# Kernel tuning notes

Measured on AMD Instinct MI355X. Metric: run time of the kernel, lower is better.

The kernel has to match this reference:

```python
import jax, jax.numpy as jnp
import numpy as np

B, C, H, W = 16, 256, 64, 64
DIM = 8
HEADS = C // DIM          # 32
TD = HEADS * DIM          # 256 (total_dim)
EPS = 1e-15
BN_EPS = 1e-5


def setup_inputs() -> dict:
    key = jax.random.key(0)
    ks = jax.random.split(key, 7)
    s = 0.05
    return {
        "x": jax.random.normal(ks[0], (B, C, H, W), jnp.float32),
        "w_qkv": jax.random.normal(ks[1], (3 * TD, C), jnp.float32) * s,
        "w_dw": jax.random.normal(ks[2], (3 * TD, 1, 5, 5), jnp.float32) * s,
        "w_pw": jax.random.normal(ks[3], (3 * TD, DIM), jnp.float32) * s,
        "w_proj": jax.random.normal(ks[4], (C, 2 * TD), jnp.float32) * s,
        "bn_gamma": jnp.ones((C,), jnp.float32),
        "bn_beta": jnp.zeros((C,), jnp.float32),
        "bn_mean": jax.random.normal(ks[5], (C,), jnp.float32) * 0.1,
        "bn_var": jax.random.uniform(ks[6], (C,), jnp.float32, 0.5, 1.5),
    }


def reference(x, w_qkv, w_dw, w_pw, w_proj, bn_gamma, bn_beta, bn_mean, bn_var):
    # qkv: 1x1 conv, no bias -> (B, 3*TD, H, W)
    qkv = jnp.einsum('bchw,oc->bohw', x, w_qkv)

    # multi-scale aggregation: 5x5 depthwise conv then grouped 1x1 conv (groups = 3*HEADS)
    dw = jax.lax.conv_general_dilated(
        qkv, w_dw, window_strides=(1, 1), padding=[(2, 2), (2, 2)],
        dimension_numbers=('NCHW', 'OIHW', 'NCHW'), feature_group_count=3 * TD)
    G = 3 * HEADS                                   # groups; DIM channels per group
    dwg = dw.reshape(B, G, DIM, H, W)
    wg = w_pw.reshape(G, DIM, DIM)                  # (group, out_per_group, in_per_group)
    agg = jnp.einsum('bgihw,goi->bgohw', dwg, wg).reshape(B, 3 * TD, H, W)

    qkv_ms = jnp.concatenate([qkv, agg], axis=1)    # (B, 6*TD, H, W)

    # ReLU linear attention (H*W > dim branch)
    h2 = qkv_ms.shape[1] // (3 * DIM)               # 2*HEADS effective heads
    t = qkv_ms.reshape(B, h2, 3 * DIM, H * W)
    q = jax.nn.relu(t[:, :, :DIM])                  # (B,h2,DIM,N)
    k = jax.nn.relu(t[:, :, DIM:2 * DIM])           # (B,h2,DIM,N)
    v = t[:, :, 2 * DIM:]                           # (B,h2,DIM,N)
    v = jnp.concatenate([v, jnp.ones_like(v[:, :, :1])], axis=2)  # pad ones row -> (B,h2,DIM+1,N)

    vk = jnp.einsum('bhen,bhdn->bhed', v, k)        # (B,h2,DIM+1,DIM)
    out = jnp.einsum('bhed,bhdn->bhen', vk, q)      # (B,h2,DIM+1,N)
    out = out[:, :, :-1] / (out[:, :, -1:] + EPS)   # normalize by padded-ones channel
    out = out.reshape(B, h2 * DIM, H, W)            # (B, 2*TD, H, W)

    # proj: 1x1 conv + BatchNorm (inference stats)
    y = jnp.einsum('bchw,oc->bohw', out, w_proj)
    scale = (bn_gamma / jnp.sqrt(bn_var + BN_EPS))[None, :, None, None]
    y = (y - bn_mean[None, :, None, None]) * scale + bn_beta[None, :, None, None]

    return x + y
```

## Files before the change

### kernel.cpp

```cpp
#include <hip/hip_runtime.h>

#define BB 16
#define CC 256
#define HW 4096
#define TD3 768
#define TD2 512
#define WQ_N (TD3 * CC)
#define WP_N (CC * TD2)

typedef __bf16 bf16x8 __attribute__((ext_vector_type(8)));
typedef float f32x4 __attribute__((ext_vector_type(4)));
typedef const __attribute__((address_space(1))) unsigned int glb_u32;
typedef __attribute__((address_space(3))) unsigned int lds_u32;

__device__ inline ushort f2bf(float f) {
    union { float f; uint u; } v; v.f = f;
    uint u = v.u;
    return (ushort)((u + 0x7FFFu + ((u >> 16) & 1u)) >> 16);
}
__device__ inline float bf2f(ushort h) {
    union { uint u; float f; } v; v.u = ((uint)h) << 16;
    return v.f;
}
__device__ inline uint pack2(float a, float b) {
    return (uint)f2bf(a) | ((uint)f2bf(b) << 16);
}

__launch_bounds__(256)
__global__ void k_prep(const float* __restrict__ w_qkv, const float* __restrict__ w_proj,
                       ushort* __restrict__ wq_hi, ushort* __restrict__ wq_lo,
                       ushort* __restrict__ wp_hi, ushort* __restrict__ wp_lo) {
    int i = blockIdx.x * 256 + threadIdx.x;
    if (i < WQ_N) {
        float f = w_qkv[i];
        ushort h = f2bf(f);
        wq_hi[i] = h;
        wq_lo[i] = f2bf(f - bf2f(h));
    }
    if (i < WP_N) {
        float f = w_proj[i];
        ushort h = f2bf(f);
        wp_hi[i] = h;
        wp_lo[i] = f2bf(f - bf2f(h));
    }
}

__launch_bounds__(256)
__global__ void k0_transpose(const float* __restrict__ x, ushort* __restrict__ x_cl) {
    __shared__ float tile[64][65];
    int b = blockIdx.z;
    int n0 = blockIdx.x * 64;
    int c0 = blockIdx.y * 64;
    int t = threadIdx.x;
    const float* xp = x + ((size_t)b * CC + c0) * HW + n0;
    int nl = t & 63;
    int cl0 = t >> 6;
#pragma unroll
    for (int i = 0; i < 16; i++) {
        int cl = cl0 + i * 4;
        tile[cl][nl] = xp[(size_t)cl * HW + nl];
    }
    __syncthreads();
#pragma unroll
    for (int it = 0; it < 2; it++) {
        int item = t + it * 256;
        int n = item >> 3;
        int cc = item & 7;
        uint4 o;
        o.x = pack2(tile[cc * 8 + 0][n], tile[cc * 8 + 1][n]);
        o.y = pack2(tile[cc * 8 + 2][n], tile[cc * 8 + 3][n]);
        o.z = pack2(tile[cc * 8 + 4][n], tile[cc * 8 + 5][n]);
        o.w = pack2(tile[cc * 8 + 6][n], tile[cc * 8 + 7][n]);
        *(uint4*)(x_cl + ((size_t)b * HW + n0 + n) * CC + c0 + cc * 8) = o;
    }
}

__launch_bounds__(256)
__global__ void k1_qkv(const ushort* __restrict__ x_cl, const ushort* __restrict__ wq_hi,
                       const ushort* __restrict__ wq_lo, ushort* __restrict__ qk_pl,
                       float* __restrict__ v_pl) {
    __shared__ ushort Ald[128][32];
    __shared__ ushort Bh[128][32];
    __shared__ ushort Bl[128][32];
    int b = blockIdx.z;
    int n0 = blockIdx.x * 128;
    int o0 = blockIdx.y * 128;
    int t = threadIdx.x;
    int w = t >> 6, l = t & 63;
    int wn = (w >> 1) * 64, wo = (w & 1) * 64;
    f32x4 acc[4][4];
#pragma unroll
    for (int m = 0; m < 4; m++)
#pragma unroll
        for (int o = 0; o < 4; o++)
#pragma unroll
            for (int r = 0; r < 4; r++) acc[m][o][r] = 0.f;

    const ushort* Ap  = x_cl + ((size_t)b * HW + n0) * CC;
    const ushort* Bph = wq_hi + (size_t)o0 * CC;
    const ushort* Bpl = wq_lo + (size_t)o0 * CC;
    int rowl = (l >> 2);
    int coll = (l & 3) * 8;

    for (int k0 = 0; k0 < CC; k0 += 32) {
#pragma unroll
        for (int i = 0; i < 2; i++) {
            int rbase = w * 32 + i * 16;
            int row = rbase + rowl;
            __builtin_amdgcn_global_load_lds((glb_u32*)(Ap + (size_t)row * CC + k0 + coll),
                                             (lds_u32*)&Ald[rbase][0], 16, 0, 0);
            __builtin_amdgcn_global_load_lds((glb_u32*)(Bph + (size_t)row * CC + k0 + coll),
                                             (lds_u32*)&Bh[rbase][0], 16, 0, 0);
            __builtin_amdgcn_global_load_lds((glb_u32*)(Bpl + (size_t)row * CC + k0 + coll),
                                             (lds_u32*)&Bl[rbase][0], 16, 0, 0);
        }
        __syncthreads();
        bf16x8 af[4], bh[4], bl[4];
#pragma unroll
        for (int m = 0; m < 4; m++) af[m] = *(const bf16x8*)&Ald[wn + m * 16 + (l & 15)][(l >> 4) * 8];
#pragma unroll
        for (int o = 0; o < 4; o++) {
            bh[o] = *(const bf16x8*)&Bh[wo + o * 16 + (l & 15)][(l >> 4) * 8];
            bl[o] = *(const bf16x8*)&Bl[wo + o * 16 + (l & 15)][(l >> 4) * 8];
        }
#pragma unroll
        for (int m = 0; m < 4; m++)
#pragma unroll
            for (int o = 0; o < 4; o++) {
                acc[m][o] = __builtin_amdgcn_mfma_f32_16x16x32_bf16(af[m], bh[o], acc[m][o], 0, 0, 0);
                acc[m][o] = __builtin_amdgcn_mfma_f32_16x16x32_bf16(af[m], bl[o], acc[m][o], 0, 0, 0);
            }
        __syncthreads();
    }
#pragma unroll
    for (int m = 0; m < 4; m++) {
        int nb = n0 + wn + m * 16 + (l >> 4) * 4;
#pragma unroll
        for (int oi = 0; oi < 4; oi++) {
            int o = o0 + wo + oi * 16 + (l & 15);
            int hl = o / 24;
            int r = o - hl * 24;
            if (r < 16) {
                uint2 pv;
                pv.x = pack2(acc[m][oi][0], acc[m][oi][1]);
                pv.y = pack2(acc[m][oi][2], acc[m][oi][3]);
                *(uint2*)(qk_pl + ((size_t)b * 1024 + hl * 16 + r) * HW + nb) = pv;
            } else {
                float4 v4 = {acc[m][oi][0], acc[m][oi][1], acc[m][oi][2], acc[m][oi][3]};
                *(float4*)(v_pl + ((size_t)b * 512 + hl * 8 + (r - 16)) * HW + nb) = v4;
            }
        }
    }
}

__launch_bounds__(256)
__global__ void k2_dwpw(ushort* __restrict__ qk_pl, float* __restrict__ v_pl,
                        const float* __restrict__ w_dw, const float* __restrict__ w_pw) {
    int g = blockIdx.x;
    int strip = blockIdx.y;
    int b = blockIdx.z;
    int t = threadIdx.x;
    int seg = t & 15, row = t >> 4;
    int y = strip * 16 + row;
    int hl = g / 3, tau = g % 3;
    const float* wg  = w_dw + (size_t)g * 200;
    const float* wpg = w_pw + (size_t)g * 64;

    float ag[8][4];
#pragma unroll
    for (int o = 0; o < 8; o++)
#pragma unroll
        for (int k = 0; k < 4; k++) ag[o][k] = 0.f;

    int xbase = 4 * seg - 2;

    if (tau < 2) {
        const ushort* src = qk_pl + ((size_t)b * 1024 + hl * 16 + tau * 8) * HW;
        ushort* dst = qk_pl + ((size_t)b * 1024 + 512 + hl * 16 + tau * 8) * HW;
#pragma unroll 1
        for (int c = 0; c < 8; c++) {
            float dw[4] = {0.f, 0.f, 0.f, 0.f};
            float win[5][8];
#pragma unroll
            for (int j = 0; j < 5; j++) {
                int yy = y - 2 + j;
#pragma unroll
                for (int i = 0; i < 8; i++) win[j][i] = 0.f;
                if (yy >= 0 && yy < 64) {
                    ushort4 wa = *(const ushort4*)(src + (size_t)c * HW + yy * 64 + xbase);
                    ushort4 wb = *(const ushort4*)(src + (size_t)c * HW + yy * 64 + xbase + 4);
                    win[j][0] = bf2f(wa.x); win[j][1] = bf2f(wa.y);
                    win[j][2] = bf2f(wa.z); win[j][3] = bf2f(wa.w);
                    win[j][4] = bf2f(wb.x); win[j][5] = bf2f(wb.y);
                    win[j][6] = bf2f(wb.z); win[j][7] = bf2f(wb.w);
                    if (seg == 0)  { win[j][0] = 0.f; win[j][1] = 0.f; }
                    if (seg == 15) { win[j][6] = 0.f; win[j][7] = 0.f; }
                }
            }
#pragma unroll
            for (int j = 0; j < 5; j++)
#pragma unroll
                for (int dx = 0; dx < 5; dx++) {
                    float wv = wg[c * 25 + j * 5 + dx];
#pragma unroll
                    for (int k = 0; k < 4; k++) dw[k] += win[j][dx + k] * wv;
                }
#pragma unroll
            for (int o = 0; o < 8; o++) {
                float wv = wpg[o * 8 + c];
#pragma unroll
                for (int k = 0; k < 4; k++) ag[o][k] += dw[k] * wv;
            }
        }
        int n = y * 64 + seg * 4;
#pragma unroll
        for (int o = 0; o < 8; o++) {
            uint2 r0;
            r0.x = pack2(ag[o][0], ag[o][1]); r0.y = pack2(ag[o][2], ag[o][3]);
            *(uint2*)(dst + (size_t)o * HW + n) = r0;
        }
    } else {
        const float* src = v_pl + ((size_t)b * 512 + hl * 8) * HW;
        float* dst = v_pl + ((size_t)b * 512 + 256 + hl * 8) * HW;
#pragma unroll 1
        for (int c = 0; c < 8; c++) {
            float dw[4] = {0.f, 0.f, 0.f, 0.f};
            float win[5][8];
#pragma unroll
            for (int j = 0; j < 5; j++) {
                int yy = y - 2 + j;
#pragma unroll
                for (int i = 0; i < 8; i++) win[j][i] = 0.f;
                if (yy >= 0 && yy < 64) {
                    float4 wa = *(const float4*)(src + (size_t)c * HW + yy * 64 + xbase);
                    float4 wb = *(const float4*)(src + (size_t)c * HW + yy * 64 + xbase + 4);
                    win[j][0] = wa.x; win[j][1] = wa.y; win[j][2] = wa.z; win[j][3] = wa.w;
                    win[j][4] = wb.x; win[j][5] = wb.y; win[j][6] = wb.z; win[j][7] = wb.w;
                    if (seg == 0)  { win[j][0] = 0.f; win[j][1] = 0.f; }
                    if (seg == 15) { win[j][6] = 0.f; win[j][7] = 0.f; }
                }
            }
#pragma unroll
            for (int j = 0; j < 5; j++)
#pragma unroll
                for (int dx = 0; dx < 5; dx++) {
                    float wv = wg[c * 25 + j * 5 + dx];
#pragma unroll
                    for (int k = 0; k < 4; k++) dw[k] += win[j][dx + k] * wv;
                }
#pragma unroll
            for (int o = 0; o < 8; o++) {
                float wv = wpg[o * 8 + c];
#pragma unroll
                for (int k = 0; k < 4; k++) ag[o][k] += dw[k] * wv;
            }
        }
        int n = y * 64 + seg * 4;
#pragma unroll
        for (int o = 0; o < 8; o++) {
            float4 r0 = {ag[o][0], ag[o][1], ag[o][2], ag[o][3]};
            *(float4*)(dst + (size_t)o * HW + n) = r0;
        }
    }
}

__launch_bounds__(256)
__global__ void k3_vk(const ushort* __restrict__ qk_pl, const float* __restrict__ v_pl,
                      float* __restrict__ vk_buf) {
    __shared__ float vk_partial[4][72];
    int h = blockIdx.x;
    int b = blockIdx.y;
    int s = blockIdx.z;
    const ushort* kp = qk_pl + ((size_t)b * 1024 + (h >> 5) * 512 + (h & 31) * 16 + 8) * HW;
    const float*  vp = v_pl  + ((size_t)b * 512  + (h >> 5) * 256 + (h & 31) * 8) * HW;
    int t = threadIdx.x;
    float vk[9][8];
#pragma unroll
    for (int e = 0; e < 9; e++)
#pragma unroll
        for (int d = 0; d < 8; d++) vk[e][d] = 0.f;

#pragma unroll
    for (int it = 0; it < 2; it++) {
        int n4 = s * 2048 + (t + it * 256) * 4;
        float4 kf[8], vf[8];
#pragma unroll
        for (int d = 0; d < 8; d++) {
            ushort4 ku = *(const ushort4*)(kp + (size_t)d * HW + n4);
            kf[d].x = fmaxf(bf2f(ku.x), 0.f); kf[d].y = fmaxf(bf2f(ku.y), 0.f);
            kf[d].z = fmaxf(bf2f(ku.z), 0.f); kf[d].w = fmaxf(bf2f(ku.w), 0.f);
        }
#pragma unroll
        for (int e = 0; e < 8; e++) vf[e] = *(const float4*)(vp + (size_t)e * HW + n4);
#pragma unroll
        for (int e = 0; e < 8; e++)
#pragma unroll
            for (int d = 0; d < 8; d++)
                vk[e][d] += vf[e].x * kf[d].x + vf[e].y * kf[d].y + vf[e].z * kf[d].z + vf[e].w * kf[d].w;
#pragma unroll
        for (int d = 0; d < 8; d++) vk[8][d] += kf[d].x + kf[d].y + kf[d].z + kf[d].w;
    }
#pragma unroll
    for (int e = 0; e < 9; e++)
#pragma unroll
        for (int d = 0; d < 8; d++) {
            float v = vk[e][d];
            for (int off = 32; off > 0; off >>= 1) v += __shfl_xor(v, off);
            vk[e][d] = v;
        }
    int w = t >> 6, l = t & 63;
    if (l == 0) {
#pragma unroll
        for (int e = 0; e < 9; e++)
#pragma unroll
            for (int d = 0; d < 8; d++) vk_partial[w][e * 8 + d] = vk[e][d];
    }
    __syncthreads();
    if (t < 72) {
        float sum = vk_partial[0][t] + vk_partial[1][t] + vk_partial[2][t] + vk_partial[3][t];
        vk_buf[(((size_t)b * 64 + h) * 2 + s) * 72 + t] = sum;
    }
}

__launch_bounds__(256)
__global__ void k3_out(const ushort* __restrict__ qk_pl, const float* __restrict__ vk_buf,
                       ushort* __restrict__ out_cl) {
    __shared__ float vk_s[72];
    int h = blockIdx.x;
    int b = blockIdx.y;
    int s = blockIdx.z;
    const ushort* qp = qk_pl + ((size_t)b * 1024 + (h >> 5) * 512 + (h & 31) * 16) * HW;
    int t = threadIdx.x;
    if (t < 72) {
        const float* vb = vk_buf + ((size_t)b * 64 + h) * 2 * 72 + t;
        vk_s[t] = vb[0] + vb[72];
    }
    __syncthreads();
    float vkf[9][8];
#pragma unroll
    for (int e = 0; e < 9; e++)
#pragma unroll
        for (int d = 0; d < 8; d++) vkf[e][d] = vk_s[e * 8 + d];

    int n4 = s * 1024 + t * 4;
    float qa[4][8];
#pragma unroll
    for (int d = 0; d < 8; d++) {
        ushort4 qu = *(const ushort4*)(qp + (size_t)d * HW + n4);
        qa[0][d] = fmaxf(bf2f(qu.x), 0.f); qa[1][d] = fmaxf(bf2f(qu.y), 0.f);
        qa[2][d] = fmaxf(bf2f(qu.z), 0.f); qa[3][d] = fmaxf(bf2f(qu.w), 0.f);
    }
    ushort* dst = out_cl + (size_t)b * HW * TD2 + h * 8;
#pragma unroll
    for (int j = 0; j < 4; j++) {
        float o[9];
#pragma unroll
        for (int e = 0; e < 9; e++) {
            float sum = 0.f;
#pragma unroll
            for (int d = 0; d < 8; d++) sum += vkf[e][d] * qa[j][d];
            o[e] = sum;
        }
        float inv = 1.f / (o[8] + 1e-15f);
        uint4 ov;
        ov.x = pack2(o[0] * inv, o[1] * inv); ov.y = pack2(o[2] * inv, o[3] * inv);
        ov.z = pack2(o[4] * inv, o[5] * inv); ov.w = pack2(o[6] * inv, o[7] * inv);
        *(uint4*)(dst + (size_t)(n4 + j) * TD2) = ov;
    }
}

__launch_bounds__(256)
__global__ void k4_proj(const ushort* __restrict__ out_cl, const ushort* __restrict__ wp_hi,
                        const ushort* __restrict__ wp_lo, const float* __restrict__ x,
                        const float* __restrict__ gamma, const float* __restrict__ beta,
                        const float* __restrict__ mean, const float* __restrict__ var_,
                        float* __restrict__ out) {
    __shared__ ushort Ah[128][32];
    __shared__ ushort Al[128][32];
    __shared__ ushort Bld[128][32];
    int b = blockIdx.z;
    int n0 = blockIdx.x * 128;
    int c0 = blockIdx.y * 128;
    int t = threadIdx.x;
    int w = t >> 6, l = t & 63;
    int wc = (w >> 1) * 64, wn = (w & 1) * 64;
    f32x4 acc[4][4];
#pragma unroll
    for (int m = 0; m < 4; m++)
#pragma unroll
        for (int o = 0; o < 4; o++)
#pragma unroll
            for (int r = 0; r < 4; r++) acc[m][o][r] = 0.f;

    const ushort* Aph = wp_hi + (size_t)c0 * TD2;
    const ushort* Apl = wp_lo + (size_t)c0 * TD2;
    const ushort* Bp  = out_cl + ((size_t)b * HW + n0) * TD2;
    int rowl = (l >> 2);
    int coll = (l & 3) * 8;

    for (int k0 = 0; k0 < TD2; k0 += 32) {
#pragma unroll
        for (int i = 0; i < 2; i++) {
            int rbase = w * 32 + i * 16;
            int row = rbase + rowl;
            __builtin_amdgcn_global_load_lds((glb_u32*)(Aph + (size_t)row * TD2 + k0 + coll),
                                             (lds_u32*)&Ah[rbase][0], 16, 0, 0);
            __builtin_amdgcn_global_load_lds((glb_u32*)(Apl + (size_t)row * TD2 + k0 + coll),
                                             (lds_u32*)&Al[rbase][0], 16, 0, 0);
            __builtin_amdgcn_global_load_lds((glb_u32*)(Bp + (size_t)row * TD2 + k0 + coll),
                                             (lds_u32*)&Bld[rbase][0], 16, 0, 0);
        }
        __syncthreads();
        bf16x8 ah[4], al[4], bf[4];
#pragma unroll
        for (int m = 0; m < 4; m++) {
            ah[m] = *(const bf16x8*)&Ah[wc + m * 16 + (l & 15)][(l >> 4) * 8];
            al[m] = *(const bf16x8*)&Al[wc + m * 16 + (l & 15)][(l >> 4) * 8];
        }
#pragma unroll
        for (int ni = 0; ni < 4; ni++) bf[ni] = *(const bf16x8*)&Bld[wn + ni * 16 + (l & 15)][(l >> 4) * 8];
#pragma unroll
        for (int m = 0; m < 4; m++)
#pragma unroll
            for (int ni = 0; ni < 4; ni++) {
                acc[m][ni] = __builtin_amdgcn_mfma_f32_16x16x32_bf16(ah[m], bf[ni], acc[m][ni], 0, 0, 0);
                acc[m][ni] = __builtin_amdgcn_mfma_f32_16x16x32_bf16(al[m], bf[ni], acc[m][ni], 0, 0, 0);
            }
        __syncthreads();
    }
#pragma unroll
    for (int m = 0; m < 4; m++) {
        int cb = c0 + wc + m * 16 + (l >> 4) * 4;
        float sc[4], mn[4], bt[4];
#pragma unroll
        for (int r = 0; r < 4; r++) {
            sc[r] = gamma[cb + r] * rsqrtf(var_[cb + r] + 1e-5f);
            mn[r] = mean[cb + r];
            bt[r] = beta[cb + r];
        }
#pragma unroll
        for (int ni = 0; ni < 4; ni++) {
            int n = n0 + wn + ni * 16 + (l & 15);
#pragma unroll
            for (int r = 0; r < 4; r++) {
                size_t idx = ((size_t)b * CC + cb + r) * HW + n;
                out[idx] = x[idx] + (acc[m][ni][r] - mn[r]) * sc[r] + bt[r];
            }
        }
    }
}

extern "C" void kernel_launch(void* const* d_in, const int* in_sizes, int n_in,
                              void* d_out, int out_size, void* d_ws, size_t ws_size,
                              hipStream_t stream) {
    const float* x      = (const float*)d_in[0];
    const float* w_qkv  = (const float*)d_in[1];
    const float* w_dw   = (const float*)d_in[2];
    const float* w_pw   = (const float*)d_in[3];
    const float* w_proj = (const float*)d_in[4];
    const float* gamma  = (const float*)d_in[5];
    const float* beta   = (const float*)d_in[6];
    const float* mean   = (const float*)d_in[7];
    const float* var_   = (const float*)d_in[8];
    float* out = (float*)d_out;

    const size_t static_bytes = ((size_t)WQ_N + WP_N) * 2 * 2;
    const size_t per_batch = (size_t)HW * CC * 2 + (size_t)1024 * HW * 2 + (size_t)512 * HW * 4
                           + (size_t)HW * TD2 * 2 + (size_t)64 * 2 * 72 * 4;
    size_t avail = ws_size > static_bytes ? ws_size - static_bytes : 0;
    int cb = 16;
    while (cb > 1 && (size_t)cb * per_batch > avail) cb >>= 1;

    char* ws = (char*)d_ws;
    ushort* x_cl  = (ushort*)ws;
    ushort* qk_pl = (ushort*)(ws + (size_t)cb * HW * CC * 2);
    float*  v_pl  = (float*)(ws + (size_t)cb * HW * CC * 2 + (size_t)cb * 1024 * HW * 2);
    ushort* out_cl = (ushort*)(ws + (size_t)cb * HW * CC * 2 + (size_t)cb * 1024 * HW * 2
                                  + (size_t)cb * 512 * HW * 4);
    float*  vk_buf = (float*)(ws + (size_t)cb * HW * CC * 2 + (size_t)cb * 1024 * HW * 2
                                 + (size_t)cb * 512 * HW * 4 + (size_t)cb * HW * TD2 * 2);
    char* wsw = ws + (size_t)cb * per_batch;
    ushort* wq_hi = (ushort*)wsw;
    ushort* wq_lo = wq_hi + WQ_N;
    ushort* wp_hi = wq_lo + WQ_N;
    ushort* wp_lo = wp_hi + WP_N;

    k_prep<<<dim3((WQ_N + 255) / 256), 256, 0, stream>>>(w_qkv, w_proj, wq_hi, wq_lo, wp_hi, wp_lo);

    for (int b0 = 0; b0 < BB; b0 += cb) {
        const float* xc = x + (size_t)b0 * CC * HW;
        float* oc = out + (size_t)b0 * CC * HW;
        k0_transpose<<<dim3(64, 4, cb), 256, 0, stream>>>(xc, x_cl);
        k1_qkv<<<dim3(32, 6, cb), 256, 0, stream>>>(x_cl, wq_hi, wq_lo, qk_pl, v_pl);
        k2_dwpw<<<dim3(96, 4, cb), 256, 0, stream>>>(qk_pl, v_pl, w_dw, w_pw);
        k3_vk<<<dim3(64, cb, 2), 256, 0, stream>>>(qk_pl, v_pl, vk_buf);
        k3_out<<<dim3(64, cb, 4), 256, 0, stream>>>(qk_pl, vk_buf, out_cl);
        k4_proj<<<dim3(32, 2, cb), 256, 0, stream>>>(out_cl, wp_hi, wp_lo, xc, gamma, beta, mean, var_, oc);
    }
}
```

Measured before the change: 410.4 us.

## Store V in bf16 in unified qkv buffer and stage depthwise input through LDS

Merges the separate bf16 q/k buffer and fp32 v buffer into a single bf16 planar qkv buffer in natural channel order. This halves the bytes written and read for v and simplifies indexing. The depthwise 5x5 plus pointwise kernel now loads a 20-row halo tile for 8 channels into shared memory with zero padding, so it no longer does redundant overlapping global loads and boundary branches. V losing fp32 precision risks accuracy, and the LDS stage adds a barrier and shared memory use.

```diff
diff --git a/kernel.cpp b/kernel.cpp
--- a/kernel.cpp
+++ b/kernel.cpp
@@ -20,6 +20,14 @@
 }
 __device__ inline float bf2f(ushort h) {
     union { uint u; float f; } v; v.u = ((uint)h) << 16;
+    return v.f;
+}
+__device__ inline float bf2f_lo(uint u) {
+    union { uint u; float f; } v; v.u = u << 16;
+    return v.f;
+}
+__device__ inline float bf2f_hi(uint u) {
+    union { uint u; float f; } v; v.u = u & 0xffff0000u;
     return v.f;
 }
 __device__ inline uint pack2(float a, float b) {
@@ -77,8 +85,7 @@
 
 __launch_bounds__(256)
 __global__ void k1_qkv(const ushort* __restrict__ x_cl, const ushort* __restrict__ wq_hi,
-                       const ushort* __restrict__ wq_lo, ushort* __restrict__ qk_pl,
-                       float* __restrict__ v_pl) {
+                       const ushort* __restrict__ wq_lo, ushort* __restrict__ qkv_pl) {
     __shared__ ushort Ald[128][32];
     __shared__ ushort Bh[128][32];
     __shared__ ushort Bl[128][32];
@@ -138,141 +145,103 @@
 #pragma unroll
         for (int oi = 0; oi < 4; oi++) {
             int o = o0 + wo + oi * 16 + (l & 15);
-            int hl = o / 24;
-            int r = o - hl * 24;
-            if (r < 16) {
-                uint2 pv;
-                pv.x = pack2(acc[m][oi][0], acc[m][oi][1]);
-                pv.y = pack2(acc[m][oi][2], acc[m][oi][3]);
-                *(uint2*)(qk_pl + ((size_t)b * 1024 + hl * 16 + r) * HW + nb) = pv;
-            } else {
-                float4 v4 = {acc[m][oi][0], acc[m][oi][1], acc[m][oi][2], acc[m][oi][3]};
-                *(float4*)(v_pl + ((size_t)b * 512 + hl * 8 + (r - 16)) * HW + nb) = v4;
-            }
-        }
-    }
-}
-
-__launch_bounds__(256)
-__global__ void k2_dwpw(ushort* __restrict__ qk_pl, float* __restrict__ v_pl,
-                        const float* __restrict__ w_dw, const float* __restrict__ w_pw) {
+            uint2 pv;
+            pv.x = pack2(acc[m][oi][0], acc[m][oi][1]);
+            pv.y = pack2(acc[m][oi][2], acc[m][oi][3]);
+            *(uint2*)(qkv_pl + ((size_t)b * 1536 + o) * HW + nb) = pv;
+        }
+    }
+}
+
+__launch_bounds__(256)
+__global__ void k2_dwpw(ushort* __restrict__ qkv_pl, const float* __restrict__ w_dw,
+                        const float* __restrict__ w_pw) {
+    __shared__ __align__(16) ushort lds[8][20][74];
     int g = blockIdx.x;
     int strip = blockIdx.y;
     int b = blockIdx.z;
     int t = threadIdx.x;
-    int seg = t & 15, row = t >> 4;
-    int y = strip * 16 + row;
-    int hl = g / 3, tau = g % 3;
+    int y0 = strip * 16;
     const float* wg  = w_dw + (size_t)g * 200;
     const float* wpg = w_pw + (size_t)g * 64;
-
+    const ushort* src = qkv_pl + ((size_t)b * 1536 + g * 8) * HW;
+    ushort* dst = qkv_pl + ((size_t)b * 1536 + 768 + g * 8) * HW;
+
+    if (t < 160) {
+        int ch = t / 20, r = t - ch * 20;
+        *(uint*)(&lds[ch][r][0]) = 0u;
+        *(uint*)(&lds[ch][r][66]) = 0u;
+    }
+#pragma unroll
+    for (int i = 0; i < 5; i++) {
+        int slot = t + i * 256;
+        int ch = slot / 160;
+        int rem = slot - ch * 160;
+        int r = rem >> 3;
+        int u = rem & 7;
+        int yy = y0 - 2 + r;
+        uint4 v = {0u, 0u, 0u, 0u};
+        if (yy >= 0 && yy < 64)
+            v = *(const uint4*)(src + (size_t)ch * HW + yy * 64 + u * 8);
+        ushort* p = &lds[ch][r][2 + u * 8];
+        *(uint*)(p + 0) = v.x; *(uint*)(p + 2) = v.y;
+        *(uint*)(p + 4) = v.z; *(uint*)(p + 6) = v.w;
+    }
+    __syncthreads();
+
+    int seg = t & 15, row = t >> 4;
     float ag[8][4];
 #pragma unroll
     for (int o = 0; o < 8; o++)
 #pragma unroll
         for (int k = 0; k < 4; k++) ag[o][k] = 0.f;
 
-    int xbase = 4 * seg - 2;
-
-    if (tau < 2) {
-        const ushort* src = qk_pl + ((size_t)b * 1024 + hl * 16 + tau * 8) * HW;
-        ushort* dst = qk_pl + ((size_t)b * 1024 + 512 + hl * 16 + tau * 8) * HW;
 #pragma unroll 1
-        for (int c = 0; c < 8; c++) {
-            float dw[4] = {0.f, 0.f, 0.f, 0.f};
-            float win[5][8];
-#pragma unroll
-            for (int j = 0; j < 5; j++) {
-                int yy = y - 2 + j;
-#pragma unroll
-                for (int i = 0; i < 8; i++) win[j][i] = 0.f;
-                if (yy >= 0 && yy < 64) {
-                    ushort4 wa = *(const ushort4*)(src + (size_t)c * HW + yy * 64 + xbase);
-                    ushort4 wb = *(const ushort4*)(src + (size_t)c * HW + yy * 64 + xbase + 4);
-                    win[j][0] = bf2f(wa.x); win[j][1] = bf2f(wa.y);
-                    win[j][2] = bf2f(wa.z); win[j][3] = bf2f(wa.w);
-                    win[j][4] = bf2f(wb.x); win[j][5] = bf2f(wb.y);
-                    win[j][6] = bf2f(wb.z); win[j][7] = bf2f(wb.w);
-                    if (seg == 0)  { win[j][0] = 0.f; win[j][1] = 0.f; }
-                    if (seg == 15) { win[j][6] = 0.f; win[j][7] = 0.f; }
-                }
+    for (int c = 0; c < 8; c++) {
+        float dw[4] = {0.f, 0.f, 0.f, 0.f};
+#pragma unroll
+        for (int j = 0; j < 5; j++) {
+            const ushort* rp = &lds[c][row + j][4 * seg];
+            uint2 a = *(const uint2*)(rp);
+            uint2 bq = *(const uint2*)(rp + 4);
+            float win[8];
+            win[0] = bf2f_lo(a.x);  win[1] = bf2f_hi(a.x);
+            win[2] = bf2f_lo(a.y);  win[3] = bf2f_hi(a.y);
+            win[4] = bf2f_lo(bq.x); win[5] = bf2f_hi(bq.x);
+            win[6] = bf2f_lo(bq.y); win[7] = bf2f_hi(bq.y);
+#pragma unroll
+            for (int dx = 0; dx < 5; dx++) {
+                float wv = wg[c * 25 + j * 5 + dx];
+#pragma unroll
+                for (int k = 0; k < 4; k++) dw[k] += win[dx + k] * wv;
             }
-#pragma unroll
-            for (int j = 0; j < 5; j++)
-#pragma unroll
-                for (int dx = 0; dx < 5; dx++) {
-                    float wv = wg[c * 25 + j * 5 + dx];
-#pragma unroll
-                    for (int k = 0; k < 4; k++) dw[k] += win[j][dx + k] * wv;
-                }
-#pragma unroll
-            for (int o = 0; o < 8; o++) {
-                float wv = wpg[o * 8 + c];
-#pragma unroll
-                for (int k = 0; k < 4; k++) ag[o][k] += dw[k] * wv;
-            }
-        }
-        int n = y * 64 + seg * 4;
+        }
 #pragma unroll
         for (int o = 0; o < 8; o++) {
-            uint2 r0;
-            r0.x = pack2(ag[o][0], ag[o][1]); r0.y = pack2(ag[o][2], ag[o][3]);
-            *(uint2*)(dst + (size_t)o * HW + n) = r0;
-        }
-    } else {
-        const float* src = v_pl + ((size_t)b * 512 + hl * 8) * HW;
-        float* dst = v_pl + ((size_t)b * 512 + 256 + hl * 8) * HW;
-#pragma unroll 1
-        for (int c = 0; c < 8; c++) {
-            float dw[4] = {0.f, 0.f, 0.f, 0.f};
-            float win[5][8];
-#pragma unroll
-            for (int j = 0; j < 5; j++) {
-                int yy = y - 2 + j;
-#pragma unroll
-                for (int i = 0; i < 8; i++) win[j][i] = 0.f;
-                if (yy >= 0 && yy < 64) {
-                    float4 wa = *(const float4*)(src + (size_t)c * HW + yy * 64 + xbase);
-                    float4 wb = *(const float4*)(src + (size_t)c * HW + yy * 64 + xbase + 4);
-                    win[j][0] = wa.x; win[j][1] = wa.y; win[j][2] = wa.z; win[j][3] = wa.w;
-                    win[j][4] = wb.x; win[j][5] = wb.y; win[j][6] = wb.z; win[j][7] = wb.w;
-                    if (seg == 0)  { win[j][0] = 0.f; win[j][1] = 0.f; }
-                    if (seg == 15) { win[j][6] = 0.f; win[j][7] = 0.f; }
-                }
-            }
-#pragma unroll
-            for (int j = 0; j < 5; j++)
-#pragma unroll
-                for (int dx = 0; dx < 5; dx++) {
-                    float wv = wg[c * 25 + j * 5 + dx];
-#pragma unroll
-                    for (int k = 0; k < 4; k++) dw[k] += win[j][dx + k] * wv;
-                }
-#pragma unroll
-            for (int o = 0; o < 8; o++) {
-                float wv = wpg[o * 8 + c];
-#pragma unroll
-                for (int k = 0; k < 4; k++) ag[o][k] += dw[k] * wv;
-            }
-        }
-        int n = y * 64 + seg * 4;
-#pragma unroll
-        for (int o = 0; o < 8; o++) {
-            float4 r0 = {ag[o][0], ag[o][1], ag[o][2], ag[o][3]};
-            *(float4*)(dst + (size_t)o * HW + n) = r0;
-        }
-    }
-}
-
-__launch_bounds__(256)
-__global__ void k3_vk(const ushort* __restrict__ qk_pl, const float* __restrict__ v_pl,
-                      float* __restrict__ vk_buf) {
+            float wv = wpg[o * 8 + c];
+#pragma unroll
+            for (int k = 0; k < 4; k++) ag[o][k] += dw[k] * wv;
+        }
+    }
+    int n = (y0 + row) * 64 + seg * 4;
+#pragma unroll
+    for (int o = 0; o < 8; o++) {
+        uint2 r0;
+        r0.x = pack2(ag[o][0], ag[o][1]);
+        r0.y = pack2(ag[o][2], ag[o][3]);
+        *(uint2*)(dst + (size_t)o * HW + n) = r0;
+    }
+}
+
+__launch_bounds__(256)
+__global__ void k3_vk(const ushort* __restrict__ qkv_pl, float* __restrict__ vk_buf) {
     __shared__ float vk_partial[4][72];
     int h = blockIdx.x;
     int b = blockIdx.y;
     int s = blockIdx.z;
-    const ushort* kp = qk_pl + ((size_t)b * 1024 + (h >> 5) * 512 + (h & 31) * 16 + 8) * HW;
-    const float*  vp = v_pl  + ((size_t)b * 512  + (h >> 5) * 256 + (h & 31) * 8) * HW;
+    size_t base = (size_t)b * 1536 + (h < 32 ? 0 : 768) + (size_t)(h & 31) * 24;
+    const ushort* kp = qkv_pl + (base + 8) * HW;
+    const ushort* vp = qkv_pl + (base + 16) * HW;
     int t = threadIdx.x;
     float vk[9][8];
 #pragma unroll
@@ -291,7 +260,11 @@
             kf[d].z = fmaxf(bf2f(ku.z), 0.f); kf[d].w = fmaxf(bf2f(ku.w), 0.f);
         }
 #pragma unroll
-        for (int e = 0; e < 8; e++) vf[e] = *(const float4*)(vp + (size_t)e * HW + n4);
+        for (int e = 0; e < 8; e++) {
+            ushort4 vu = *(const ushort4*)(vp + (size_t)e * HW + n4);
+            vf[e].x = bf2f(vu.x); vf[e].y = bf2f(vu.y);
+            vf[e].z = bf2f(vu.z); vf[e].w = bf2f(vu.w);
+        }
 #pragma unroll
         for (int e = 0; e < 8; e++)
 #pragma unroll
@@ -323,13 +296,14 @@
 }
 
 __launch_bounds__(256)
-__global__ void k3_out(const ushort* __restrict__ qk_pl, const float* __restrict__ vk_buf,
+__global__ void k3_out(const ushort* __restrict__ qkv_pl, const float* __restrict__ vk_buf,
                        ushort* __restrict__ out_cl) {
     __shared__ float vk_s[72];
     int h = blockIdx.x;
     int b = blockIdx.y;
     int s = blockIdx.z;
-    const ushort* qp = qk_pl + ((size_t)b * 1024 + (h >> 5) * 512 + (h & 31) * 16) * HW;
+    size_t base = (size_t)b * 1536 + (h < 32 ? 0 : 768) + (size_t)(h & 31) * 24;
+    const ushort* qp = qkv_pl + base * HW;
     int t = threadIdx.x;
     if (t < 72) {
         const float* vb = vk_buf + ((size_t)b * 64 + h) * 2 * 72 + t;
@@ -465,20 +439,18 @@
     float* out = (float*)d_out;
 
     const size_t static_bytes = ((size_t)WQ_N + WP_N) * 2 * 2;
-    const size_t per_batch = (size_t)HW * CC * 2 + (size_t)1024 * HW * 2 + (size_t)512 * HW * 4
+    const size_t per_batch = (size_t)HW * CC * 2 + (size_t)1536 * HW * 2
                            + (size_t)HW * TD2 * 2 + (size_t)64 * 2 * 72 * 4;
     size_t avail = ws_size > static_bytes ? ws_size - static_bytes : 0;
     int cb = 16;
     while (cb > 1 && (size_t)cb * per_batch > avail) cb >>= 1;
 
     char* ws = (char*)d_ws;
-    ushort* x_cl  = (ushort*)ws;
-    ushort* qk_pl = (ushort*)(ws + (size_t)cb * HW * CC * 2);
-    float*  v_pl  = (float*)(ws + (size_t)cb * HW * CC * 2 + (size_t)cb * 1024 * HW * 2);
-    ushort* out_cl = (ushort*)(ws + (size_t)cb * HW * CC * 2 + (size_t)cb * 1024 * HW * 2
-                                  + (size_t)cb * 512 * HW * 4);
-    float*  vk_buf = (float*)(ws + (size_t)cb * HW * CC * 2 + (size_t)cb * 1024 * HW * 2
-                                 + (size_t)cb * 512 * HW * 4 + (size_t)cb * HW * TD2 * 2);
+    ushort* x_cl   = (ushort*)ws;
+    ushort* qkv_pl = (ushort*)(ws + (size_t)cb * HW * CC * 2);
+    ushort* out_cl = (ushort*)(ws + (size_t)cb * HW * CC * 2 + (size_t)cb * 1536 * HW * 2);
+    float*  vk_buf = (float*)(ws + (size_t)cb * HW * CC * 2 + (size_t)cb * 1536 * HW * 2
+                                 + (size_t)cb * HW * TD2 * 2);
     char* wsw = ws + (size_t)cb * per_batch;
     ushort* wq_hi = (ushort*)wsw;
     ushort* wq_lo = wq_hi + WQ_N;
@@ -491,10 +463,10 @@
         const float* xc = x + (size_t)b0 * CC * HW;
         float* oc = out + (size_t)b0 * CC * HW;
         k0_transpose<<<dim3(64, 4, cb), 256, 0, stream>>>(xc, x_cl);
-        k1_qkv<<<dim3(32, 6, cb), 256, 0, stream>>>(x_cl, wq_hi, wq_lo, qk_pl, v_pl);
-        k2_dwpw<<<dim3(96, 4, cb), 256, 0, stream>>>(qk_pl, v_pl, w_dw, w_pw);
-        k3_vk<<<dim3(64, cb, 2), 256, 0, stream>>>(qk_pl, v_pl, vk_buf);
-        k3_out<<<dim3(64, cb, 4), 256, 0, stream>>>(qk_pl, vk_buf, out_cl);
+        k1_qkv<<<dim3(32, 6, cb), 256, 0, stream>>>(x_cl, wq_hi, wq_lo, qkv_pl);
+        k2_dwpw<<<dim3(96, 4, cb), 256, 0, stream>>>(qkv_pl, w_dw, w_pw);
+        k3_vk<<<dim3(64, cb, 2), 256, 0, stream>>>(qkv_pl, vk_buf);
+        k3_out<<<dim3(64, cb, 4), 256, 0, stream>>>(qkv_pl, vk_buf, out_cl);
         k4_proj<<<dim3(32, 2, cb), 256, 0, stream>>>(out_cl, wp_hi, wp_lo, xc, gamma, beta, mean, var_, oc);
     }
 }
```

Measured after the change: 481.6 us. +17.3%, slower.
